# Kernel tuning notes

Measured on AMD Instinct MI355X. Metric: run time of the kernel, lower is better.

Reference implementation:

```python
import jax, jax.numpy as jnp
import numpy as np

N = 50000      # num_nodes
E = 800000     # num_edges (before self loops)
EMB = 128      # emb_dim
GH = 64        # gcn_hidden
TD = 4         # temporal_dim
B = 64         # batch of sequences
T = 200        # max sequence length
H = 128        # lstm_hidden (per direction)
IN_DIM = 2 + EMB + TD


def lstm_scan(x_tbi, w_ih, w_hh, b_ih, b_hh):
    """x_tbi: [T, B, I] -> hidden states [T, B, H]. PyTorch gate order i,f,g,o."""
    Bsz = x_tbi.shape[1]
    Hh = w_hh.shape[1]

    def step(carry, xt):
        h, c = carry
        g = xt @ w_ih.T + h @ w_hh.T + b_ih + b_hh
        i, f, gg, o = jnp.split(g, 4, axis=-1)
        c = jax.nn.sigmoid(f) * c + jax.nn.sigmoid(i) * jnp.tanh(gg)
        h = jax.nn.sigmoid(o) * jnp.tanh(c)
        return (h, c), h

    init = (jnp.zeros((Bsz, Hh), x_tbi.dtype), jnp.zeros((Bsz, Hh), x_tbi.dtype))
    _, hs = jax.lax.scan(step, init, x_tbi)
    return hs


def gcn_layer(x, W, b, src, dst, ew):
    """PyG GCNConv: linear -> symmetric-norm gather/scatter-add -> bias.
    (self loops already appended to src/dst/ew by caller)"""
    h = x @ W  # [N, out]
    deg = jax.ops.segment_sum(ew, dst, num_segments=N)
    dinv = jnp.where(deg > 0, jax.lax.rsqrt(deg), 0.0)
    norm = dinv[src] * ew * dinv[dst]            # [E+N]
    msg = h[src] * norm[:, None]                  # gather + scale
    return jax.ops.segment_sum(msg, dst, num_segments=N) + b


def setup_inputs() -> dict:
    key = jax.random.key(0)
    ks = jax.random.split(key, 16)
    s = 0.02
    return {
        'x_coords': jax.random.normal(ks[0], (N, 2), jnp.float32),
        'temporal_features': jax.random.uniform(ks[1], (N, TD), jnp.float32, -1.0, 1.0),
        'edge_index': jax.random.randint(ks[2], (2, E), 0, N),
        'edge_weight': jnp.ones((E,), jnp.float32),
        'seq': jax.random.randint(ks[3], (B, T), 0, N),
        'lengths': jax.random.randint(ks[4], (B,), 1, T + 1),
        'node_emb': jax.random.normal(ks[5], (N, EMB), jnp.float32) * s,
        'gcn1_w': jax.random.normal(ks[6], (IN_DIM, GH), jnp.float32) * s,
        'gcn1_b': jnp.zeros((GH,), jnp.float32),
        'gcn2_w': jax.random.normal(ks[7], (GH, EMB), jnp.float32) * s,
        'gcn2_b': jnp.zeros((EMB,), jnp.float32),
        'w_ih_f': jax.random.normal(ks[8], (4 * H, EMB), jnp.float32) * s,
        'w_hh_f': jax.random.normal(ks[9], (4 * H, H), jnp.float32) * s,
        'b_ih_f': jnp.zeros((4 * H,), jnp.float32),
        'b_hh_f': jnp.zeros((4 * H,), jnp.float32),
        'w_ih_b': jax.random.normal(ks[10], (4 * H, EMB), jnp.float32) * s,
        'w_hh_b': jax.random.normal(ks[11], (4 * H, H), jnp.float32) * s,
        'b_ih_b': jnp.zeros((4 * H,), jnp.float32),
        'b_hh_b': jnp.zeros((4 * H,), jnp.float32),
        'attn_w': jax.random.normal(ks[12], (2 * H,), jnp.float32) * s,
        'attn_b': jnp.zeros((), jnp.float32),
        'fc_w': jax.random.normal(ks[13], (2 * H, N), jnp.float32) * s,
        'fc_b': jnp.zeros((N,), jnp.float32),
    }


def reference(x_coords, temporal_features, edge_index, edge_weight, seq, lengths,
              node_emb, gcn1_w, gcn1_b, gcn2_w, gcn2_b,
              w_ih_f, w_hh_f, b_ih_f, b_hh_f,
              w_ih_b, w_hh_b, b_ih_b, b_hh_b,
              attn_w, attn_b, fc_w, fc_b):
    # --- GCN with self loops (PyG add_self_loops=True, fill_value=1) ---
    loop = jnp.arange(N)
    src = jnp.concatenate([edge_index[0], loop])
    dst = jnp.concatenate([edge_index[1], loop])
    ew = jnp.concatenate([edge_weight, jnp.ones((N,), edge_weight.dtype)])

    x = jnp.concatenate([x_coords, node_emb, temporal_features], axis=1)  # [N, 134]
    z = jax.nn.relu(gcn_layer(x, gcn1_w, gcn1_b, src, dst, ew))
    z = gcn_layer(z, gcn2_w, gcn2_b, src, dst, ew)  # dropout = identity (eval)

    # --- sequence embedding + BiLSTM ---
    seq_emb = z[seq]                                  # [B, T, EMB]
    h_f = lstm_scan(seq_emb.transpose(1, 0, 2), w_ih_f, w_hh_f, b_ih_f, b_hh_f)
    h_f = h_f.transpose(1, 0, 2)                      # [B, T, H]

    # backward direction: reverse each sequence within its valid length
    t = jnp.arange(T)
    valid = t[None, :] < lengths[:, None]             # [B, T]
    rev_idx = jnp.where(valid, lengths[:, None] - 1 - t[None, :], t[None, :])
    x_rev = jnp.take_along_axis(seq_emb, rev_idx[:, :, None], axis=1)
    h_b = lstm_scan(x_rev.transpose(1, 0, 2), w_ih_b, w_hh_b, b_ih_b, b_hh_b)
    h_b = jnp.take_along_axis(h_b.transpose(1, 0, 2), rev_idx[:, :, None], axis=1)

    lstm_out = jnp.concatenate([h_f, h_b], axis=-1)   # [B, T, 2H]

    # --- masked attention pooling ---
    scores = lstm_out @ attn_w + attn_b               # [B, T]
    scores = jnp.where(valid, scores, -jnp.inf)
    aw = jax.nn.softmax(scores, axis=1)
    context = jnp.einsum('bt,btd->bd', aw, lstm_out)  # [B, 2H]

    return context @ fc_w + fc_b                      # [B, N]
```

## Files before the change

### kernel.cpp

```cpp
#include <hip/hip_runtime.h>
#include <math.h>

#define NN 50000
#define NE 800000
#define EMB 128
#define GH 64
#define BB 64
#define TT 200
#define HH 128
#define G4 512
#define IND 134
#define PM 128
#define PO 128

__device__ __forceinline__ float sigf(float x) { return 1.0f / (1.0f + __expf(-x)); }
__device__ __forceinline__ float tanhf_(float x) { return 1.0f - 2.0f / (__expf(2.0f * x) + 1.0f); }
__device__ __forceinline__ void fma4(float4& a, float s, const float4 w) {
    a.x += s * w.x; a.y += s * w.y; a.z += s * w.z; a.w += s * w.w;
}

__global__ void hist_kernel(const int* __restrict__ ei, const float* __restrict__ ew,
                            int* __restrict__ cnt, float* __restrict__ degw) {
    int e = blockIdx.x * 256 + threadIdx.x;
    if (e >= NE) return;
    int d = ei[NE + e];
    atomicAdd(&cnt[d], 1);
    atomicAdd(&degw[d], ew[e]);
}

__global__ void dinv_kernel(const float* __restrict__ degw, float* __restrict__ dinv) {
    int n = blockIdx.x * 256 + threadIdx.x;
    if (n >= NN) return;
    dinv[n] = rsqrtf(degw[n] + 1.0f);
}

__global__ __launch_bounds__(1024) void scan1_kernel(const int* __restrict__ cnt,
                                                     int* __restrict__ rs, int* __restrict__ partials) {
    __shared__ int s[1024];
    int gid = blockIdx.x * 1024 + threadIdx.x;
    int v = (gid < NN) ? cnt[gid] : 0;
    s[threadIdx.x] = v;
    __syncthreads();
    for (int off = 1; off < 1024; off <<= 1) {
        int add = (threadIdx.x >= (unsigned)off) ? s[threadIdx.x - off] : 0;
        __syncthreads();
        s[threadIdx.x] += add;
        __syncthreads();
    }
    if (gid < NN) rs[gid] = s[threadIdx.x] - v;
    if (threadIdx.x == 1023) partials[blockIdx.x] = s[1023];
}

__global__ void scan2_kernel(int* __restrict__ partials, int nblk) {
    if (threadIdx.x == 0) {
        int acc = 0;
        for (int i = 0; i < nblk; ++i) { int v = partials[i]; partials[i] = acc; acc += v; }
    }
}

__global__ __launch_bounds__(1024) void scan3_kernel(const int* __restrict__ partials,
                                                     int* __restrict__ rs, int* __restrict__ cursor) {
    int gid = blockIdx.x * 1024 + threadIdx.x;
    if (gid < NN) {
        int v = rs[gid] + partials[gid >> 10];
        rs[gid] = v;
        cursor[gid] = v;
    }
    if (gid == 0) rs[NN] = NE;
}

__global__ void fill_kernel(const int* __restrict__ ei, const float* __restrict__ ew,
                            const float* __restrict__ dinv, int* __restrict__ cursor,
                            int* __restrict__ ssrc, float* __restrict__ sw) {
    int e = blockIdx.x * 256 + threadIdx.x;
    if (e >= NE) return;
    int s = ei[e], d = ei[NE + e];
    int pos = atomicAdd(&cursor[d], 1);
    ssrc[pos] = s;
    sw[pos] = ew[e] * dinv[s] * dinv[d];
}

__global__ void w1t_kernel(const float* __restrict__ W1, float* __restrict__ w1t) {
    int i = blockIdx.x * 256 + threadIdx.x;
    if (i >= 64 * 136) return;
    int o = i / 136, j = i - (i / 136) * 136;
    float v = 0.0f;
    if (j < 128) v = W1[(size_t)(j + 2) * GH + o];
    else if (j < 130) v = W1[(size_t)(j - 128) * GH + o];
    else if (j < 134) v = W1[(size_t)j * GH + o];
    w1t[i] = v;
}

__global__ __launch_bounds__(256) void gemm1_kernel(const float* __restrict__ coords,
                                                    const float* __restrict__ temporal,
                                                    const float* __restrict__ emb,
                                                    const float* __restrict__ w1t,
                                                    float* __restrict__ h1) {
    __shared__ __align__(16) float xs[128][136];
    __shared__ __align__(16) float wt[64][136];
    int tid = threadIdx.x;
    int m0 = blockIdx.x * 128;
    for (int i = tid; i < 64 * 34; i += 256) {
        int rr = i / 34, w = i - rr * 34;
        float4 v = *(const float4*)&w1t[(size_t)rr * 136 + w * 4];
        int ws = (w < 32) ? (w ^ ((rr >> 3) & 7)) : w;
        *(float4*)&wt[rr][ws * 4] = v;
    }
    for (int i = tid; i < 128 * 32; i += 256) {
        int r = i >> 5, c4 = i & 31;
        int m = m0 + r;
        float4 v = make_float4(0.f, 0.f, 0.f, 0.f);
        if (m < NN) v = *(const float4*)&emb[(size_t)m * EMB + c4 * 4];
        *(float4*)&xs[r][(c4 ^ ((r >> 2) & 7)) * 4] = v;
    }
    for (int i = tid; i < 128 * 8; i += 256) {
        int r = i >> 3, c = i & 7;
        int m = m0 + r;
        float v = 0.0f;
        if (m < NN) {
            if (c < 2) v = coords[2 * m + c];
            else if (c < 6) v = temporal[4 * m + (c - 2)];
        }
        xs[r][128 + c] = v;
    }
    __syncthreads();
    int mt = tid >> 3, ot = tid & 7;
    int xswz = mt & 7, wswz = ot & 7;
    float acc[4][8];
#pragma unroll
    for (int mi = 0; mi < 4; ++mi)
#pragma unroll
        for (int oi = 0; oi < 8; ++oi) acc[mi][oi] = 0.0f;
    for (int k4 = 0; k4 < 34; ++k4) {
        int xk = (k4 < 32) ? (k4 ^ xswz) : k4;
        int wk = (k4 < 32) ? (k4 ^ wswz) : k4;
        float4 xv[4], wv[8];
#pragma unroll
        for (int mi = 0; mi < 4; ++mi) xv[mi] = *(const float4*)&xs[mt * 4 + mi][xk * 4];
#pragma unroll
        for (int oi = 0; oi < 8; ++oi) wv[oi] = *(const float4*)&wt[ot * 8 + oi][wk * 4];
#pragma unroll
        for (int mi = 0; mi < 4; ++mi)
#pragma unroll
            for (int oi = 0; oi < 8; ++oi)
                acc[mi][oi] += xv[mi].x * wv[oi].x + xv[mi].y * wv[oi].y
                             + xv[mi].z * wv[oi].z + xv[mi].w * wv[oi].w;
    }
#pragma unroll
    for (int mi = 0; mi < 4; ++mi) {
        int m = m0 + mt * 4 + mi;
        if (m >= NN) continue;
        int ob = ot * 8;
        float4 oa = make_float4(acc[mi][0], acc[mi][1], acc[mi][2], acc[mi][3]);
        float4 obv = make_float4(acc[mi][4], acc[mi][5], acc[mi][6], acc[mi][7]);
        *(float4*)&h1[(size_t)m * GH + ob] = oa;
        *(float4*)&h1[(size_t)m * GH + ob + 4] = obv;
    }
}

__global__ __launch_bounds__(256) void agg_kernel(const float* __restrict__ hin,
                                                  const int* __restrict__ rs,
                                                  const int* __restrict__ ssrc,
                                                  const float* __restrict__ sw,
                                                  const float* __restrict__ dinv,
                                                  const float* __restrict__ bias, int relu,
                                                  float* __restrict__ hout) {
    int lane = threadIdx.x & 63;
    int wid = threadIdx.x >> 6;
    int n = blockIdx.x * 4 + wid;
    if (n >= NN) return;
    float dv = dinv[n];
    float acc = hin[(size_t)n * GH + lane] * (dv * dv);
    int i = rs[n], e1 = rs[n + 1];
    for (; i + 3 < e1; i += 4) {
        int s0 = ssrc[i], s1 = ssrc[i + 1], s2 = ssrc[i + 2], s3 = ssrc[i + 3];
        float w0 = sw[i], w1 = sw[i + 1], w2 = sw[i + 2], w3 = sw[i + 3];
        float a0 = hin[(size_t)s0 * GH + lane];
        float a1 = hin[(size_t)s1 * GH + lane];
        float a2 = hin[(size_t)s2 * GH + lane];
        float a3 = hin[(size_t)s3 * GH + lane];
        acc += a0 * w0 + a1 * w1 + a2 * w2 + a3 * w3;
    }
    for (; i < e1; ++i) acc += hin[(size_t)ssrc[i] * GH + lane] * sw[i];
    if (bias) acc += bias[lane];
    if (relu) acc = fmaxf(acc, 0.0f);
    hout[(size_t)n * GH + lane] = acc;
}

__global__ void w2t_kernel(const float* __restrict__ W2, float* __restrict__ w2t) {
    int i = blockIdx.x * 256 + threadIdx.x;
    if (i >= GH * EMB) return;
    int o = i >> 6, k = i & 63;
    w2t[i] = W2[(size_t)k * EMB + o];
}

__global__ __launch_bounds__(256) void gemm2_kernel(const float* __restrict__ a2,
                                                    const float* __restrict__ w2t,
                                                    const float* __restrict__ b2,
                                                    float* __restrict__ z2) {
    int m0 = blockIdx.x * 128, o0 = blockIdx.y * 64;
    __shared__ __align__(16) float xs[128][64];
    __shared__ __align__(16) float wt[64][64];
    __shared__ float bsh[64];
    int tid = threadIdx.x;
#pragma unroll
    for (int i = 0; i < 8; ++i) {
        int idx = i * 256 + tid;
        int r = idx >> 4, c4 = idx & 15;
        int m = m0 + r;
        float4 v = (m < NN) ? *(const float4*)&a2[(size_t)m * GH + c4 * 4]
                            : make_float4(0.f, 0.f, 0.f, 0.f);
        *(float4*)&xs[r][(c4 ^ ((r >> 2) & 3)) * 4] = v;
    }
#pragma unroll
    for (int i = 0; i < 4; ++i) {
        int idx = i * 256 + tid;
        int r = idx >> 4, c4 = idx & 15;
        float4 v = *(const float4*)&w2t[(size_t)(o0 + r) * GH + c4 * 4];
        *(float4*)&wt[r][(c4 ^ ((r >> 3) & 7)) * 4] = v;
    }
    if (tid < 64) bsh[tid] = b2[o0 + tid];
    __syncthreads();
    int mt = tid >> 3, ot = tid & 7;
    float acc[4][8];
#pragma unroll
    for (int mi = 0; mi < 4; ++mi)
#pragma unroll
        for (int oi = 0; oi < 8; ++oi) acc[mi][oi] = 0.0f;
    for (int k4 = 0; k4 < 16; ++k4) {
        int xc = (k4 ^ (mt & 3)) * 4;
        int wc = (k4 ^ (ot & 7)) * 4;
        float4 xv[4], wv[8];
#pragma unroll
        for (int mi = 0; mi < 4; ++mi) xv[mi] = *(const float4*)&xs[mt * 4 + mi][xc];
#pragma unroll
        for (int oi = 0; oi < 8; ++oi) wv[oi] = *(const float4*)&wt[ot * 8 + oi][wc];
#pragma unroll
        for (int mi = 0; mi < 4; ++mi)
#pragma unroll
            for (int oi = 0; oi < 8; ++oi)
                acc[mi][oi] += xv[mi].x * wv[oi].x + xv[mi].y * wv[oi].y
                             + xv[mi].z * wv[oi].z + xv[mi].w * wv[oi].w;
    }
#pragma unroll
    for (int mi = 0; mi < 4; ++mi) {
        int m = m0 + mt * 4 + mi;
        if (m >= NN) continue;
        int ob = ot * 8;
        float4 oa = make_float4(acc[mi][0] + bsh[ob + 0], acc[mi][1] + bsh[ob + 1],
                                acc[mi][2] + bsh[ob + 2], acc[mi][3] + bsh[ob + 3]);
        float4 obv = make_float4(acc[mi][4] + bsh[ob + 4], acc[mi][5] + bsh[ob + 5],
                                 acc[mi][6] + bsh[ob + 6], acc[mi][7] + bsh[ob + 7]);
        *(float4*)&z2[(size_t)m * EMB + o0 + ob] = oa;
        *(float4*)&z2[(size_t)m * EMB + o0 + ob + 4] = obv;
    }
}

__global__ void gather_kernel(const int* __restrict__ seq, const float* __restrict__ z2,
                              float* __restrict__ se) {
    int idx = blockIdx.x * 256 + threadIdx.x;
    if (idx >= BB * TT * 32) return;
    int r = idx >> 5, q = idx & 31;
    int node = seq[r];
    ((float4*)se)[(size_t)r * 32 + q] = ((const float4*)z2)[(size_t)node * 32 + q];
}

__global__ __launch_bounds__(256) void pregemm_kernel(const float* __restrict__ se,
                                                      const float* __restrict__ w_ih_f,
                                                      const float* __restrict__ w_ih_b,
                                                      const float* __restrict__ b_ih_f,
                                                      const float* __restrict__ b_hh_f,
                                                      const float* __restrict__ b_ih_b,
                                                      const float* __restrict__ b_hh_b,
                                                      const int* __restrict__ lengths,
                                                      float* __restrict__ xpf,
                                                      float* __restrict__ xpb) {
    int dir = blockIdx.z;
    const float* w_ih = dir ? w_ih_b : w_ih_f;
    int o0 = blockIdx.y * PO;
    int m0 = blockIdx.x * PM;
    __shared__ __align__(16) float xs[PM][EMB];
    __shared__ __align__(16) float ws[PO][EMB];
    __shared__ float bsh[PO];
    int tid = threadIdx.x;
#pragma unroll
    for (int i = 0; i < 16; ++i) {
        int idx = i * 256 + tid;
        int row = idx >> 5, c4 = idx & 31;
        float4 v = *(const float4*)&w_ih[(size_t)(o0 + row) * EMB + c4 * 4];
        *(float4*)&ws[row][(c4 ^ ((row >> 3) & 7)) * 4] = v;
    }
    if (tid < PO) bsh[tid] = dir ? (b_ih_b[o0 + tid] + b_hh_b[o0 + tid])
                                 : (b_ih_f[o0 + tid] + b_hh_f[o0 + tid]);
#pragma unroll
    for (int i = 0; i < 16; ++i) {
        int idx = i * 256 + tid;
        int r = idx >> 5, c4 = idx & 31;
        int m = m0 + r;
        int t = m >> 6, b = m & 63;
        int tsrc = t;
        if (dir) { int len = lengths[b]; tsrc = (t < len) ? (len - 1 - t) : t; }
        float4 v = *(const float4*)&se[((size_t)b * TT + tsrc) * EMB + c4 * 4];
        *(float4*)&xs[r][(c4 ^ ((r >> 3) & 3)) * 4] = v;
    }
    __syncthreads();
    int mt = tid >> 4, ot = tid & 15;
    int mswz = mt & 3, oswz = ot & 7;
    float acc[8][8];
#pragma unroll
    for (int mi = 0; mi < 8; ++mi)
#pragma unroll
        for (int oi = 0; oi < 8; ++oi) acc[mi][oi] = 0.0f;
    for (int k4 = 0; k4 < 32; ++k4) {
        int xk = (k4 ^ mswz) * 4;
        int wk = (k4 ^ oswz) * 4;
        float4 xv[8], wv[8];
#pragma unroll
        for (int mi = 0; mi < 8; ++mi) xv[mi] = *(const float4*)&xs[mt * 8 + mi][xk];
#pragma unroll
        for (int oi = 0; oi < 8; ++oi) wv[oi] = *(const float4*)&ws[ot * 8 + oi][wk];
#pragma unroll
        for (int mi = 0; mi < 8; ++mi)
#pragma unroll
            for (int oi = 0; oi < 8; ++oi)
                acc[mi][oi] += xv[mi].x * wv[oi].x + xv[mi].y * wv[oi].y
                             + xv[mi].z * wv[oi].z + xv[mi].w * wv[oi].w;
    }
    float* xp = dir ? xpb : xpf;
#pragma unroll
    for (int mi = 0; mi < 8; ++mi) {
        int m = m0 + mt * 8 + mi;
        int ob = ot * 8;
        float4 oa = make_float4(acc[mi][0] + bsh[ob + 0], acc[mi][1] + bsh[ob + 1],
                                acc[mi][2] + bsh[ob + 2], acc[mi][3] + bsh[ob + 3]);
        float4 obv = make_float4(acc[mi][4] + bsh[ob + 4], acc[mi][5] + bsh[ob + 5],
                                 acc[mi][6] + bsh[ob + 6], acc[mi][7] + bsh[ob + 7]);
        *(float4*)&xp[(size_t)m * G4 + o0 + ob] = oa;
        *(float4*)&xp[(size_t)m * G4 + o0 + ob + 4] = obv;
    }
}

__global__ __launch_bounds__(1024, 4) void lstm_kernel(const float* __restrict__ xpf,
                                                       const float* __restrict__ xpb,
                                                       const float* __restrict__ w_hh_f,
                                                       const float* __restrict__ w_hh_b,
                                                       const int* __restrict__ lengths,
                                                       float* __restrict__ hfo,
                                                       float* __restrict__ hbo) {
    int chain = blockIdx.x;
    int dir = chain & 1, b = chain >> 1;
    const float* w_hh = dir ? w_hh_b : w_hh_f;
    const float* xp = dir ? xpb : xpf;
    float* ho = dir ? hbo : hfo;
    int tid = threadIdx.x;
    int u = tid & 127;
    int kq = tid >> 7;
    int len = lengths[b];

    float4 W[4][4];
#pragma unroll
    for (int g = 0; g < 4; ++g)
#pragma unroll
        for (int j4 = 0; j4 < 4; ++j4)
            W[g][j4] = *(const float4*)&w_hh[(size_t)(g * HH + u) * HH + kq * 16 + j4 * 4];

    __shared__ __align__(16) float hl[HH];
    __shared__ __align__(16) float part[HH][9][4];
    if (tid < HH) hl[tid] = 0.0f;
    __syncthreads();

    float cst = 0.0f;
    float x0 = 0.f, x1 = 0.f, x2 = 0.f, x3 = 0.f;
    const float* xpt = xp + (size_t)b * G4 + u;
    if (tid < HH && len > 0) {
        x0 = xpt[0]; x1 = xpt[HH]; x2 = xpt[2 * HH]; x3 = xpt[3 * HH];
    }
    for (int t = 0; t < len; ++t) {
        const float4* h4 = (const float4*)&hl[kq * 16];
        float a0 = 0.f, a1 = 0.f, a2 = 0.f, a3 = 0.f;
#pragma unroll
        for (int j4 = 0; j4 < 4; ++j4) {
            float4 hv = h4[j4];
            a0 += W[0][j4].x * hv.x + W[0][j4].y * hv.y + W[0][j4].z * hv.z + W[0][j4].w * hv.w;
            a1 += W[1][j4].x * hv.x + W[1][j4].y * hv.y + W[1][j4].z * hv.z + W[1][j4].w * hv.w;
            a2 += W[2][j4].x * hv.x + W[2][j4].y * hv.y + W[2][j4].z * hv.z + W[2][j4].w * hv.w;
            a3 += W[3][j4].x * hv.x + W[3][j4].y * hv.y + W[3][j4].z * hv.z + W[3][j4].w * hv.w;
        }
        if (kq) *(float4*)&part[u][kq][0] = make_float4(a0, a1, a2, a3);
        __syncthreads();
        if (tid < HH) {
            float n0 = 0.f, n1 = 0.f, n2 = 0.f, n3 = 0.f;
            if (t + 1 < len) {
                const float* xn = xpt + (size_t)(t + 1) * (BB * G4);
                n0 = xn[0]; n1 = xn[HH]; n2 = xn[2 * HH]; n3 = xn[3 * HH];
            }
            float s0 = x0 + a0, s1 = x1 + a1, s2 = x2 + a2, s3 = x3 + a3;
#pragma unroll
            for (int q = 1; q < 8; ++q) {
                float4 p = *(const float4*)&part[u][q][0];
                s0 += p.x; s1 += p.y; s2 += p.z; s3 += p.w;
            }
            float gi = sigf(s0), gf = sigf(s1), gg = tanhf_(s2), go = sigf(s3);
            cst = gf * cst + gi * gg;
            float h = go * tanhf_(cst);
            hl[u] = h;
            int tt = dir ? (len - 1 - t) : t;
            ho[((size_t)b * TT + tt) * HH + u] = h;
            x0 = n0; x1 = n1; x2 = n2; x3 = n3;
        }
        __syncthreads();
    }
}

__global__ __launch_bounds__(256) void attn_kernel(const float* __restrict__ hf,
                                                   const float* __restrict__ hb,
                                                   const float* __restrict__ attn_w,
                                                   const float* __restrict__ attn_b,
                                                   const int* __restrict__ lengths,
                                                   float* __restrict__ ctx) {
    int b = blockIdx.x;
    int tid = threadIdx.x;
    int len = lengths[b];
    __shared__ __align__(16) float wl[256];
    __shared__ float pl[256];
    __shared__ float red[256];
    wl[tid] = attn_w[tid];
    __syncthreads();
    float sc = -3.0e38f;
    if (tid < len) {
        const float4* rf = (const float4*)(hf + ((size_t)b * TT + tid) * HH);
        const float4* rb = (const float4*)(hb + ((size_t)b * TT + tid) * HH);
        const float4* w4 = (const float4*)wl;
        float s = attn_b[0];
        for (int k4 = 0; k4 < 32; ++k4) {
            float4 a = rf[k4], ww = w4[k4];
            s += a.x * ww.x + a.y * ww.y + a.z * ww.z + a.w * ww.w;
        }
        for (int k4 = 0; k4 < 32; ++k4) {
            float4 a = rb[k4], ww = w4[32 + k4];
            s += a.x * ww.x + a.y * ww.y + a.z * ww.z + a.w * ww.w;
        }
        sc = s;
    }
    red[tid] = sc;
    __syncthreads();
    for (int off = 128; off > 0; off >>= 1) {
        if (tid < off) red[tid] = fmaxf(red[tid], red[tid + off]);
        __syncthreads();
    }
    float mx = red[0];
    __syncthreads();
    float e = (tid < len) ? __expf(sc - mx) : 0.0f;
    red[tid] = e;
    __syncthreads();
    for (int off = 128; off > 0; off >>= 1) {
        if (tid < off) red[tid] += red[tid + off];
        __syncthreads();
    }
    float inv = 1.0f / red[0];
    pl[tid] = e * inv;
    __syncthreads();
    float acc = 0.0f;
    const float* basep = (tid < HH) ? (hf + (size_t)b * TT * HH + tid)
                                    : (hb + (size_t)b * TT * HH + (tid - HH));
#pragma unroll 4
    for (int t = 0; t < len; ++t) acc += pl[t] * basep[(size_t)t * HH];
    ctx[(size_t)b * 256 + tid] = acc;
}

__global__ __launch_bounds__(256) void fc_kernel(const float* __restrict__ ctx,
                                                 const float* __restrict__ fc_w,
                                                 const float* __restrict__ fc_b,
                                                 float* __restrict__ out) {
    __shared__ __align__(16) float cl[64][256];
    for (int i = threadIdx.x; i < 64 * 256 / 4; i += 256)
        ((float4*)cl)[i] = ((const float4*)ctx)[i];
    __syncthreads();
    int lane = threadIdx.x & 63;
    int bq = threadIdx.x >> 6;
    int nb = blockIdx.x * 256 + lane;
    float acc[16][4];
#pragma unroll
    for (int i = 0; i < 16; ++i)
#pragma unroll
        for (int c = 0; c < 4; ++c) acc[i][c] = 0.0f;
    for (int k4 = 0; k4 < 64; ++k4) {
        int k = k4 * 4;
        float w[4][4];
#pragma unroll
        for (int j = 0; j < 4; ++j)
#pragma unroll
            for (int c = 0; c < 4; ++c) {
                int n = nb + c * 64;
                w[j][c] = (n < NN) ? fc_w[(size_t)(k + j) * NN + n] : 0.0f;
            }
#pragma unroll
        for (int i = 0; i < 16; ++i) {
            float4 cv = *(const float4*)&cl[bq * 16 + i][k];
#pragma unroll
            for (int c = 0; c < 4; ++c)
                acc[i][c] += cv.x * w[0][c] + cv.y * w[1][c] + cv.z * w[2][c] + cv.w * w[3][c];
        }
    }
    float fb[4];
#pragma unroll
    for (int c = 0; c < 4; ++c) {
        int n = nb + c * 64;
        fb[c] = (n < NN) ? fc_b[n] : 0.0f;
    }
#pragma unroll
    for (int i = 0; i < 16; ++i)
#pragma unroll
        for (int c = 0; c < 4; ++c) {
            int n = nb + c * 64;
            if (n < NN) out[(size_t)(bq * 16 + i) * NN + n] = acc[i][c] + fb[c];
        }
}

extern "C" void kernel_launch(void* const* d_in, const int* in_sizes, int n_in,
                              void* d_out, int out_size, void* d_ws, size_t ws_size,
                              hipStream_t stream) {
    const float* x_coords   = (const float*)d_in[0];
    const float* temporal   = (const float*)d_in[1];
    const int*   edge_index = (const int*)d_in[2];
    const float* edge_w     = (const float*)d_in[3];
    const int*   seq        = (const int*)d_in[4];
    const int*   lengths    = (const int*)d_in[5];
    const float* node_emb   = (const float*)d_in[6];
    const float* gcn1_w     = (const float*)d_in[7];
    const float* gcn1_b     = (const float*)d_in[8];
    const float* gcn2_w     = (const float*)d_in[9];
    const float* gcn2_b     = (const float*)d_in[10];
    const float* w_ih_f     = (const float*)d_in[11];
    const float* w_hh_f     = (const float*)d_in[12];
    const float* b_ih_f     = (const float*)d_in[13];
    const float* b_hh_f     = (const float*)d_in[14];
    const float* w_ih_b     = (const float*)d_in[15];
    const float* w_hh_b     = (const float*)d_in[16];
    const float* b_ih_b     = (const float*)d_in[17];
    const float* b_hh_b     = (const float*)d_in[18];
    const float* attn_w     = (const float*)d_in[19];
    const float* attn_b     = (const float*)d_in[20];
    const float* fc_w       = (const float*)d_in[21];
    const float* fc_b       = (const float*)d_in[22];
    float* out = (float*)d_out;

    char* base = (char*)d_ws;
    size_t off = 0;
    auto alloc = [&](size_t nbytes) -> void* {
        void* p = base + off;
        off = (off + nbytes + 255) & ~(size_t)255;
        return p;
    };
    int*   cnt     = (int*)alloc((size_t)2 * NN * 4);
    float* degw    = (float*)(cnt + NN);
    float* dinv    = (float*)alloc((size_t)NN * 4);
    int*   rs      = (int*)alloc(((size_t)NN + 1) * 4);
    int*   cursor  = (int*)alloc((size_t)NN * 4);
    int*   partials= (int*)alloc(64 * 4);
    int*   ssrc    = (int*)alloc((size_t)NE * 4);
    float* sw      = (float*)alloc((size_t)NE * 4);
    float* h1      = (float*)alloc((size_t)NN * GH * 4);
    float* z1      = (float*)alloc((size_t)NN * GH * 4);
    float* a2      = h1;
    float* w1t     = (float*)alloc((size_t)64 * 136 * 4);
    float* w2t     = (float*)alloc((size_t)GH * EMB * 4);
    float* z2      = (float*)alloc((size_t)NN * EMB * 4);
    float* se      = (float*)alloc((size_t)BB * TT * EMB * 4);
    float* xpf     = (float*)alloc((size_t)TT * BB * G4 * 4);
    float* xpb     = (float*)alloc((size_t)TT * BB * G4 * 4);
    float* hfo     = (float*)alloc((size_t)BB * TT * HH * 4);
    float* hbo     = (float*)alloc((size_t)BB * TT * HH * 4);
    float* ctx     = (float*)alloc((size_t)BB * 256 * 4);
    (void)ws_size; (void)in_sizes; (void)n_in; (void)out_size;

    hipMemsetAsync(cnt, 0, (size_t)2 * NN * 4, stream);

    hist_kernel<<<(NE + 255) / 256, 256, 0, stream>>>(edge_index, edge_w, cnt, degw);
    dinv_kernel<<<(NN + 255) / 256, 256, 0, stream>>>(degw, dinv);
    const int nblk = (NN + 1023) / 1024;
    scan1_kernel<<<nblk, 1024, 0, stream>>>(cnt, rs, partials);
    scan2_kernel<<<1, 64, 0, stream>>>(partials, nblk);
    scan3_kernel<<<nblk, 1024, 0, stream>>>(partials, rs, cursor);
    fill_kernel<<<(NE + 255) / 256, 256, 0, stream>>>(edge_index, edge_w, dinv, cursor, ssrc, sw);
    w1t_kernel<<<(64 * 136 + 255) / 256, 256, 0, stream>>>(gcn1_w, w1t);
    w2t_kernel<<<(GH * EMB + 255) / 256, 256, 0, stream>>>(gcn2_w, w2t);

    gemm1_kernel<<<(NN + 127) / 128, 256, 0, stream>>>(x_coords, temporal, node_emb, w1t, h1);
    agg_kernel<<<(NN + 3) / 4, 256, 0, stream>>>(h1, rs, ssrc, sw, dinv, gcn1_b, 1, z1);
    agg_kernel<<<(NN + 3) / 4, 256, 0, stream>>>(z1, rs, ssrc, sw, dinv, (const float*)nullptr, 0, a2);
    gemm2_kernel<<<dim3((NN + 127) / 128, 2), 256, 0, stream>>>(a2, w2t, gcn2_b, z2);

    gather_kernel<<<(BB * TT * 32 + 255) / 256, 256, 0, stream>>>(seq, z2, se);
    pregemm_kernel<<<dim3(TT * BB / PM, G4 / PO, 2), 256, 0, stream>>>(
        se, w_ih_f, w_ih_b, b_ih_f, b_hh_f, b_ih_b, b_hh_b, lengths, xpf, xpb);
    lstm_kernel<<<BB * 2, 1024, 0, stream>>>(xpf, xpb, w_hh_f, w_hh_b, lengths, hfo, hbo);
    attn_kernel<<<BB, 256, 0, stream>>>(hfo, hbo, attn_w, attn_b, lengths, ctx);
    fc_kernel<<<(NN + 255) / 256, 256, 0, stream>>>(ctx, fc_w, fc_b, out);
}
```

Baseline: 673.6 us.

## Fuse small setup kernels, pack edge src/weight, fuse gather into pregemm, tweak LSTM and FC

Several unrelated changes. The dinv computation moves into the first scan kernel, and the partial scan and weight transposes are merged into one multi-role kernel to cut launches. The separate source and weight arrays for the CSR edges are packed into one int2 array so the aggregation reads both with vector loads. The sequence gather is folded into the pregemm load. In the LSTM, the next-step input prefetch and the previous step's output store move ahead of the recurrent matmul. In the FC kernel, the shared-memory staging of the context is dropped in favour of direct, wave-uniform global reads.

```diff
diff --git a/kernel.cpp b/kernel.cpp
--- a/kernel.cpp
+++ b/kernel.cpp
@@ -15,9 +15,6 @@
 
 __device__ __forceinline__ float sigf(float x) { return 1.0f / (1.0f + __expf(-x)); }
 __device__ __forceinline__ float tanhf_(float x) { return 1.0f - 2.0f / (__expf(2.0f * x) + 1.0f); }
-__device__ __forceinline__ void fma4(float4& a, float s, const float4 w) {
-    a.x += s * w.x; a.y += s * w.y; a.z += s * w.z; a.w += s * w.w;
-}
 
 __global__ void hist_kernel(const int* __restrict__ ei, const float* __restrict__ ew,
                             int* __restrict__ cnt, float* __restrict__ degw) {
@@ -28,17 +25,14 @@
     atomicAdd(&degw[d], ew[e]);
 }
 
-__global__ void dinv_kernel(const float* __restrict__ degw, float* __restrict__ dinv) {
-    int n = blockIdx.x * 256 + threadIdx.x;
-    if (n >= NN) return;
-    dinv[n] = rsqrtf(degw[n] + 1.0f);
-}
-
 __global__ __launch_bounds__(1024) void scan1_kernel(const int* __restrict__ cnt,
+                                                     const float* __restrict__ degw,
+                                                     float* __restrict__ dinv,
                                                      int* __restrict__ rs, int* __restrict__ partials) {
     __shared__ int s[1024];
     int gid = blockIdx.x * 1024 + threadIdx.x;
     int v = (gid < NN) ? cnt[gid] : 0;
+    if (gid < NN) dinv[gid] = rsqrtf(degw[gid] + 1.0f);
     s[threadIdx.x] = v;
     __syncthreads();
     for (int off = 1; off < 1024; off <<= 1) {
@@ -51,10 +45,39 @@
     if (threadIdx.x == 1023) partials[blockIdx.x] = s[1023];
 }
 
-__global__ void scan2_kernel(int* __restrict__ partials, int nblk) {
-    if (threadIdx.x == 0) {
-        int acc = 0;
-        for (int i = 0; i < nblk; ++i) { int v = partials[i]; partials[i] = acc; acc += v; }
+__global__ void misc_kernel(int* __restrict__ partials, int nblk,
+                            const float* __restrict__ W1, float* __restrict__ w1t,
+                            const float* __restrict__ W2, float* __restrict__ w2t) {
+    int blk = blockIdx.x;
+    int tid = threadIdx.x;
+    if (blk == 0) {
+        __shared__ int s[64];
+        int v = (tid < nblk) ? partials[tid] : 0;
+        s[tid] = v;
+        __syncthreads();
+        for (int off = 1; off < 64; off <<= 1) {
+            int add = (tid >= off) ? s[tid - off] : 0;
+            __syncthreads();
+            s[tid] += add;
+            __syncthreads();
+        }
+        if (tid < nblk) partials[tid] = s[tid] - v;
+    } else if (blk <= 34) {
+        int i = (blk - 1) * 256 + tid;
+        if (i < 64 * 136) {
+            int o = i / 136, j = i - o * 136;
+            float v = 0.0f;
+            if (j < 128) v = W1[(size_t)(j + 2) * GH + o];
+            else if (j < 130) v = W1[(size_t)(j - 128) * GH + o];
+            else if (j < 134) v = W1[(size_t)j * GH + o];
+            w1t[i] = v;
+        }
+    } else {
+        int i = (blk - 35) * 256 + tid;
+        if (i < GH * EMB) {
+            int o = i >> 6, k = i & 63;
+            w2t[i] = W2[(size_t)k * EMB + o];
+        }
     }
 }
 
@@ -71,24 +94,12 @@
 
 __global__ void fill_kernel(const int* __restrict__ ei, const float* __restrict__ ew,
                             const float* __restrict__ dinv, int* __restrict__ cursor,
-                            int* __restrict__ ssrc, float* __restrict__ sw) {
+                            int2* __restrict__ ssrcw) {
     int e = blockIdx.x * 256 + threadIdx.x;
     if (e >= NE) return;
     int s = ei[e], d = ei[NE + e];
     int pos = atomicAdd(&cursor[d], 1);
-    ssrc[pos] = s;
-    sw[pos] = ew[e] * dinv[s] * dinv[d];
-}
-
-__global__ void w1t_kernel(const float* __restrict__ W1, float* __restrict__ w1t) {
-    int i = blockIdx.x * 256 + threadIdx.x;
-    if (i >= 64 * 136) return;
-    int o = i / 136, j = i - (i / 136) * 136;
-    float v = 0.0f;
-    if (j < 128) v = W1[(size_t)(j + 2) * GH + o];
-    else if (j < 130) v = W1[(size_t)(j - 128) * GH + o];
-    else if (j < 134) v = W1[(size_t)j * GH + o];
-    w1t[i] = v;
+    ssrcw[pos] = make_int2(s, __float_as_int(ew[e] * dinv[s] * dinv[d]));
 }
 
 __global__ __launch_bounds__(256) void gemm1_kernel(const float* __restrict__ coords,
@@ -151,17 +162,14 @@
         int m = m0 + mt * 4 + mi;
         if (m >= NN) continue;
         int ob = ot * 8;
-        float4 oa = make_float4(acc[mi][0], acc[mi][1], acc[mi][2], acc[mi][3]);
-        float4 obv = make_float4(acc[mi][4], acc[mi][5], acc[mi][6], acc[mi][7]);
-        *(float4*)&h1[(size_t)m * GH + ob] = oa;
-        *(float4*)&h1[(size_t)m * GH + ob + 4] = obv;
+        *(float4*)&h1[(size_t)m * GH + ob] = make_float4(acc[mi][0], acc[mi][1], acc[mi][2], acc[mi][3]);
+        *(float4*)&h1[(size_t)m * GH + ob + 4] = make_float4(acc[mi][4], acc[mi][5], acc[mi][6], acc[mi][7]);
     }
 }
 
 __global__ __launch_bounds__(256) void agg_kernel(const float* __restrict__ hin,
                                                   const int* __restrict__ rs,
-                                                  const int* __restrict__ ssrc,
-                                                  const float* __restrict__ sw,
+                                                  const int2* __restrict__ ssrcw,
                                                   const float* __restrict__ dinv,
                                                   const float* __restrict__ bias, int relu,
                                                   float* __restrict__ hout) {
@@ -173,25 +181,22 @@
     float acc = hin[(size_t)n * GH + lane] * (dv * dv);
     int i = rs[n], e1 = rs[n + 1];
     for (; i + 3 < e1; i += 4) {
-        int s0 = ssrc[i], s1 = ssrc[i + 1], s2 = ssrc[i + 2], s3 = ssrc[i + 3];
-        float w0 = sw[i], w1 = sw[i + 1], w2 = sw[i + 2], w3 = sw[i + 3];
-        float a0 = hin[(size_t)s0 * GH + lane];
-        float a1 = hin[(size_t)s1 * GH + lane];
-        float a2 = hin[(size_t)s2 * GH + lane];
-        float a3 = hin[(size_t)s3 * GH + lane];
-        acc += a0 * w0 + a1 * w1 + a2 * w2 + a3 * w3;
-    }
-    for (; i < e1; ++i) acc += hin[(size_t)ssrc[i] * GH + lane] * sw[i];
+        int4 p0 = *(const int4*)&ssrcw[i];
+        int4 p1 = *(const int4*)&ssrcw[i + 2];
+        float a0 = hin[(size_t)p0.x * GH + lane];
+        float a1 = hin[(size_t)p0.z * GH + lane];
+        float a2 = hin[(size_t)p1.x * GH + lane];
+        float a3 = hin[(size_t)p1.z * GH + lane];
+        acc += a0 * __int_as_float(p0.y) + a1 * __int_as_float(p0.w)
+             + a2 * __int_as_float(p1.y) + a3 * __int_as_float(p1.w);
+    }
+    for (; i < e1; ++i) {
+        int2 p = ssrcw[i];
+        acc += hin[(size_t)p.x * GH + lane] * __int_as_float(p.y);
+    }
     if (bias) acc += bias[lane];
     if (relu) acc = fmaxf(acc, 0.0f);
     hout[(size_t)n * GH + lane] = acc;
-}
-
-__global__ void w2t_kernel(const float* __restrict__ W2, float* __restrict__ w2t) {
-    int i = blockIdx.x * 256 + threadIdx.x;
-    if (i >= GH * EMB) return;
-    int o = i >> 6, k = i & 63;
-    w2t[i] = W2[(size_t)k * EMB + o];
 }
 
 __global__ __launch_bounds__(256) void gemm2_kernel(const float* __restrict__ a2,
@@ -256,16 +261,8 @@
     }
 }
 
-__global__ void gather_kernel(const int* __restrict__ seq, const float* __restrict__ z2,
-                              float* __restrict__ se) {
-    int idx = blockIdx.x * 256 + threadIdx.x;
-    if (idx >= BB * TT * 32) return;
-    int r = idx >> 5, q = idx & 31;
-    int node = seq[r];
-    ((float4*)se)[(size_t)r * 32 + q] = ((const float4*)z2)[(size_t)node * 32 + q];
-}
-
-__global__ __launch_bounds__(256) void pregemm_kernel(const float* __restrict__ se,
+__global__ __launch_bounds__(256) void pregemm_kernel(const float* __restrict__ z2,
+                                                      const int* __restrict__ seq,
                                                       const float* __restrict__ w_ih_f,
                                                       const float* __restrict__ w_ih_b,
                                                       const float* __restrict__ b_ih_f,
@@ -300,7 +297,8 @@
         int t = m >> 6, b = m & 63;
         int tsrc = t;
         if (dir) { int len = lengths[b]; tsrc = (t < len) ? (len - 1 - t) : t; }
-        float4 v = *(const float4*)&se[((size_t)b * TT + tsrc) * EMB + c4 * 4];
+        int node = seq[b * TT + tsrc];
+        float4 v = *(const float4*)&z2[(size_t)node * EMB + c4 * 4];
         *(float4*)&xs[r][(c4 ^ ((r >> 3) & 3)) * 4] = v;
     }
     __syncthreads();
@@ -369,13 +367,22 @@
     if (tid < HH) hl[tid] = 0.0f;
     __syncthreads();
 
-    float cst = 0.0f;
+    float cst = 0.0f, hkeep = 0.0f;
+    int tprev = -1;
     float x0 = 0.f, x1 = 0.f, x2 = 0.f, x3 = 0.f;
     const float* xpt = xp + (size_t)b * G4 + u;
     if (tid < HH && len > 0) {
         x0 = xpt[0]; x1 = xpt[HH]; x2 = xpt[2 * HH]; x3 = xpt[3 * HH];
     }
     for (int t = 0; t < len; ++t) {
+        float n0 = 0.f, n1 = 0.f, n2 = 0.f, n3 = 0.f;
+        if (tid < HH) {
+            if (tprev >= 0) ho[((size_t)b * TT + tprev) * HH + u] = hkeep;
+            if (t + 1 < len) {
+                const float* xn = xpt + (size_t)(t + 1) * (BB * G4);
+                n0 = xn[0]; n1 = xn[HH]; n2 = xn[2 * HH]; n3 = xn[3 * HH];
+            }
+        }
         const float4* h4 = (const float4*)&hl[kq * 16];
         float a0 = 0.f, a1 = 0.f, a2 = 0.f, a3 = 0.f;
 #pragma unroll
@@ -389,11 +396,6 @@
         if (kq) *(float4*)&part[u][kq][0] = make_float4(a0, a1, a2, a3);
         __syncthreads();
         if (tid < HH) {
-            float n0 = 0.f, n1 = 0.f, n2 = 0.f, n3 = 0.f;
-            if (t + 1 < len) {
-                const float* xn = xpt + (size_t)(t + 1) * (BB * G4);
-                n0 = xn[0]; n1 = xn[HH]; n2 = xn[2 * HH]; n3 = xn[3 * HH];
-            }
             float s0 = x0 + a0, s1 = x1 + a1, s2 = x2 + a2, s3 = x3 + a3;
 #pragma unroll
             for (int q = 1; q < 8; ++q) {
@@ -404,12 +406,13 @@
             cst = gf * cst + gi * gg;
             float h = go * tanhf_(cst);
             hl[u] = h;
-            int tt = dir ? (len - 1 - t) : t;
-            ho[((size_t)b * TT + tt) * HH + u] = h;
+            hkeep = h;
+            tprev = dir ? (len - 1 - t) : t;
             x0 = n0; x1 = n1; x2 = n2; x3 = n3;
         }
         __syncthreads();
     }
+    if (tid < HH && tprev >= 0) ho[((size_t)b * TT + tprev) * HH + u] = hkeep;
 }
 
 __global__ __launch_bounds__(256) void attn_kernel(const float* __restrict__ hf,
@@ -472,12 +475,9 @@
                                                  const float* __restrict__ fc_w,
                                                  const float* __restrict__ fc_b,
                                                  float* __restrict__ out) {
-    __shared__ __align__(16) float cl[64][256];
-    for (int i = threadIdx.x; i < 64 * 256 / 4; i += 256)
-        ((float4*)cl)[i] = ((const float4*)ctx)[i];
-    __syncthreads();
     int lane = threadIdx.x & 63;
-    int bq = threadIdx.x >> 6;
+    int bq = __builtin_amdgcn_readfirstlane(threadIdx.x >> 6);
+    const float* cb = ctx + (size_t)bq * 16 * 256;
     int nb = blockIdx.x * 256 + lane;
     float acc[16][4];
 #pragma unroll
@@ -496,24 +496,18 @@
             }
 #pragma unroll
         for (int i = 0; i < 16; ++i) {
-            float4 cv = *(const float4*)&cl[bq * 16 + i][k];
+            float4 cv = *(const float4*)&cb[i * 256 + k];
 #pragma unroll
             for (int c = 0; c < 4; ++c)
                 acc[i][c] += cv.x * w[0][c] + cv.y * w[1][c] + cv.z * w[2][c] + cv.w * w[3][c];
         }
     }
-    float fb[4];
-#pragma unroll
-    for (int c = 0; c < 4; ++c) {
-        int n = nb + c * 64;
-        fb[c] = (n < NN) ? fc_b[n] : 0.0f;
-    }
 #pragma unroll
     for (int i = 0; i < 16; ++i)
 #pragma unroll
         for (int c = 0; c < 4; ++c) {
             int n = nb + c * 64;
-            if (n < NN) out[(size_t)(bq * 16 + i) * NN + n] = acc[i][c] + fb[c];
+            if (n < NN) out[(size_t)(bq * 16 + i) * NN + n] = acc[i][c] + fc_b[n];
         }
 }
 
@@ -558,15 +552,13 @@
     int*   rs      = (int*)alloc(((size_t)NN + 1) * 4);
     int*   cursor  = (int*)alloc((size_t)NN * 4);
     int*   partials= (int*)alloc(64 * 4);
-    int*   ssrc    = (int*)alloc((size_t)NE * 4);
-    float* sw      = (float*)alloc((size_t)NE * 4);
+    int2*  ssrcw   = (int2*)alloc((size_t)NE * 8);
     float* h1      = (float*)alloc((size_t)NN * GH * 4);
     float* z1      = (float*)alloc((size_t)NN * GH * 4);
     float* a2      = h1;
     float* w1t     = (float*)alloc((size_t)64 * 136 * 4);
     float* w2t     = (float*)alloc((size_t)GH * EMB * 4);
     float* z2      = (float*)alloc((size_t)NN * EMB * 4);
-    float* se      = (float*)alloc((size_t)BB * TT * EMB * 4);
     float* xpf     = (float*)alloc((size_t)TT * BB * G4 * 4);
     float* xpb     = (float*)alloc((size_t)TT * BB * G4 * 4);
     float* hfo     = (float*)alloc((size_t)BB * TT * HH * 4);
@@ -577,23 +569,19 @@
     hipMemsetAsync(cnt, 0, (size_t)2 * NN * 4, stream);
 
     hist_kernel<<<(NE + 255) / 256, 256, 0, stream>>>(edge_index, edge_w, cnt, degw);
-    dinv_kernel<<<(NN + 255) / 256, 256, 0, stream>>>(degw, dinv);
     const int nblk = (NN + 1023) / 1024;
-    scan1_kernel<<<nblk, 1024, 0, stream>>>(cnt, rs, partials);
-    scan2_kernel<<<1, 64, 0, stream>>>(partials, nblk);
+    scan1_kernel<<<nblk, 1024, 0, stream>>>(cnt, degw, dinv, rs, partials);
+    misc_kernel<<<67, 256, 0, stream>>>(partials, nblk, gcn1_w, w1t, gcn2_w, w2t);
     scan3_kernel<<<nblk, 1024, 0, stream>>>(partials, rs, cursor);
-    fill_kernel<<<(NE + 255) / 256, 256, 0, stream>>>(edge_index, edge_w, dinv, cursor, ssrc, sw);
-    w1t_kernel<<<(64 * 136 + 255) / 256, 256, 0, stream>>>(gcn1_w, w1t);
-    w2t_kernel<<<(GH * EMB + 255) / 256, 256, 0, stream>>>(gcn2_w, w2t);
+    fill_kernel<<<(NE + 255) / 256, 256, 0, stream>>>(edge_index, edge_w, dinv, cursor, ssrcw);
 
     gemm1_kernel<<<(NN + 127) / 128, 256, 0, stream>>>(x_coords, temporal, node_emb, w1t, h1);
-    agg_kernel<<<(NN + 3) / 4, 256, 0, stream>>>(h1, rs, ssrc, sw, dinv, gcn1_b, 1, z1);
-    agg_kernel<<<(NN + 3) / 4, 256, 0, stream>>>(z1, rs, ssrc, sw, dinv, (const float*)nullptr, 0, a2);
+    agg_kernel<<<(NN + 3) / 4, 256, 0, stream>>>(h1, rs, ssrcw, dinv, gcn1_b, 1, z1);
+    agg_kernel<<<(NN + 3) / 4, 256, 0, stream>>>(z1, rs, ssrcw, dinv, (const float*)nullptr, 0, a2);
     gemm2_kernel<<<dim3((NN + 127) / 128, 2), 256, 0, stream>>>(a2, w2t, gcn2_b, z2);
 
-    gather_kernel<<<(BB * TT * 32 + 255) / 256, 256, 0, stream>>>(seq, z2, se);
     pregemm_kernel<<<dim3(TT * BB / PM, G4 / PO, 2), 256, 0, stream>>>(
-        se, w_ih_f, w_ih_b, b_ih_f, b_hh_f, b_ih_b, b_hh_b, lengths, xpf, xpb);
+        z2, seq, w_ih_f, w_ih_b, b_ih_f, b_hh_f, b_ih_b, b_hh_b, lengths, xpf, xpb);
     lstm_kernel<<<BB * 2, 1024, 0, stream>>>(xpf, xpb, w_hh_f, w_hh_b, lengths, hfo, hbo);
     attn_kernel<<<BB, 256, 0, stream>>>(hfo, hbo, attn_w, attn_b, lengths, ctx);
     fc_kernel<<<(NN + 255) / 256, 256, 0, stream>>>(ctx, fc_w, fc_b, out);
```

Result: no change. 666.6 us (-1.0%).
